# Optimization experiments

Hardware: AMD Instinct MI355X
Metric: run time of the kernel (lower is better)

The kernel has to match this reference:

```python
import jax, jax.numpy as jnp
import numpy as np

EPS_MASK = 1e-6   # clamp eps from DNN_Beamformer __init__
EPS_MVDR = 1e-15  # eps in get_mvdr_vector / psd normalization
SCALING = 2.0     # AttentionReference softmax scaling


def _psd(xs, mask):
    # xs: (B,F,C,T) complex, mask: (B,F,C,T) real -> psd: (B,F,C,C) complex
    m = mask.mean(axis=-2)                                   # (B,F,T)
    m = m / (m.sum(axis=-1, keepdims=True) + EPS_MVDR)
    # sum_t xs[c,t] * conj(xs[e,t]) * m[t], never materializing (B,F,T,C,C)
    return jnp.einsum('bfct,bfet,bft->bfce', xs, xs.conj(), m)


def _attention_reference(psd_in, mlp_w, mlp_b, gvec_w, gvec_b):
    # psd_in: (B,F,C,C) complex -> u: (B,C)
    C = psd_in.shape[-1]
    eye = jnp.eye(C, dtype=bool)
    psd = jnp.where(eye, 0.0, psd_in)                        # zero diagonal
    psd = psd.sum(axis=-1) / (C - 1)                         # (B,F,C)
    psd = jnp.swapaxes(psd, -1, -2)                          # (B,C,F)
    feat = jnp.sqrt(psd.real ** 2 + psd.imag ** 2)           # (B,C,F)
    h = jnp.tanh(feat @ mlp_w + mlp_b)                       # (B,C,att)
    e = (h @ gvec_w + gvec_b)[..., 0]                        # (B,C)
    return jax.nn.softmax(SCALING * e, axis=-1)


def _mvdr_vector(psd_s, psd_n, u):
    # psd_s, psd_n: (B,F,C,C) complex; u: (B,C) real -> ws: (B,F,C) complex
    C = psd_n.shape[-1]
    psd_n = psd_n + EPS_MVDR * jnp.eye(C, dtype=psd_n.dtype)
    numerator = jnp.linalg.solve(psd_n, psd_s)               # inv(psd_n) @ psd_s
    tr = jnp.trace(numerator, axis1=-2, axis2=-1)            # (B,F)
    ws = numerator / (tr[..., None, None] + EPS_MVDR)        # (B,F,C,C)
    return jnp.einsum('bfec,bc->bfe', ws, u.astype(ws.dtype))


def setup_inputs() -> dict:
    key = jax.random.key(0)
    ks = jax.random.split(key, 8)
    B, T, C, F, A = 8, 800, 8, 513, 320
    return {
        'data_real': jax.random.normal(ks[0], (B, T, C, F), jnp.float32),
        'data_imag': jax.random.normal(ks[1], (B, T, C, F), jnp.float32),
        'mask_speech': jax.random.uniform(ks[2], (B, F, C, T), jnp.float32),
        'mask_noise': jax.random.uniform(ks[3], (B, F, C, T), jnp.float32),
        'mlp_w': jax.random.normal(ks[4], (F, A), jnp.float32) / np.sqrt(F),
        'mlp_b': jnp.zeros((A,), jnp.float32),
        'gvec_w': jax.random.normal(ks[5], (A, 1), jnp.float32) / np.sqrt(A),
        'gvec_b': jnp.zeros((1,), jnp.float32),
        'ilens': jnp.full((8,), 800, dtype=jnp.int32),
    }


def reference(data_real, data_imag, mask_speech, mask_noise,
              mlp_w, mlp_b, gvec_w, gvec_b, ilens):
    # data: (B,T,C,F) -> permuted to (B,F,C,T) as in forward
    data = data_real + 1j * data_imag
    x = jnp.transpose(data, (0, 3, 2, 1))                    # (B,F,C,T)
    ms = jnp.maximum(mask_speech, EPS_MASK)
    mn = jnp.maximum(mask_noise, EPS_MASK)
    psd_s = _psd(x, ms)                                      # (B,F,C,C)
    psd_n = _psd(x, mn)                                      # (B,F,C,C)
    u = _attention_reference(psd_s, mlp_w, mlp_b, gvec_w, gvec_b)  # (B,C)
    ws = _mvdr_vector(psd_s, psd_n, u)                       # (B,F,C)
    enhanced = jnp.einsum('bfc,bfct->bft', ws.conj(), x)     # (B,F,T)
    enhanced = jnp.swapaxes(enhanced, -1, -2)                # (B,T,F)
    # return real/imag stacked so the output is a real tensor
    return jnp.stack([enhanced.real, enhanced.imag], axis=-1)
```

## Files before the change

kernel.cpp:

```cpp
#include <hip/hip_runtime.h>
#include <math.h>

#define NB 8
#define NT 800
#define NC 8
#define NF 513
#define NFT 9
#define NTC 16
#define TCHUNK 50
#define NE 146
#define NPAIR 36


__global__ __launch_bounds__(256)
void k_maskred(const float* __restrict__ ms, const float* __restrict__ mn,
               float* __restrict__ mrs, float* __restrict__ mrn) {
  __shared__ float ts[64][65];
  __shared__ float tn[64][65];
  const int tx = threadIdx.x & 63;
  const int wy = threadIdx.x >> 6;
  const int ft = blockIdx.x, tt = blockIdx.y, b = blockIdx.z;
  const int f0 = ft * 64, t0 = tt * 64;
  const int t = t0 + tx;
  const bool tvalid = (t < NT);

  for (int fl = wy; fl < 64; fl += 4) {
    const int f = f0 + fl;
    float as = 0.f, an = 0.f;
    if (f < NF && tvalid) {
      const float* mbs = ms + (((size_t)b * NF + f) * NC) * NT + t;
      const float* mbn = mn + (((size_t)b * NF + f) * NC) * NT + t;
#pragma unroll
      for (int c = 0; c < NC; c++) {
        as += fmaxf(mbs[c * NT], 1e-6f);
        an += fmaxf(mbn[c * NT], 1e-6f);
      }
    }
    ts[fl][tx] = as * 0.125f;
    tn[fl][tx] = an * 0.125f;
  }
  __syncthreads();
  for (int tl = wy; tl < 64; tl += 4) {
    const int tg = t0 + tl, f = f0 + tx;
    if (tg < NT && f < NF) {
      mrs[((size_t)b * NT + tg) * NF + f] = ts[tx][tl];
      mrn[((size_t)b * NT + tg) * NF + f] = tn[tx][tl];
    }
  }
}

__device__ __forceinline__ void accum_psd(const float* __restrict__ drb,
                                          const float* __restrict__ dib, int t,
                                          float m_s, float m_n,
                                          float* __restrict__ sr, float* __restrict__ si,
                                          float* __restrict__ nr, float* __restrict__ ni) {
  float xr[NC], xi[NC];
#pragma unroll
  for (int c = 0; c < NC; c++) {
    xr[c] = drb[(t * NC + c) * NF];
    xi[c] = dib[(t * NC + c) * NF];
  }
  int p = 0;
#pragma unroll
  for (int c = 0; c < NC; c++) {
#pragma unroll
    for (int e = c; e < NC; e++) {
      float pr = xr[c] * xr[e] + xi[c] * xi[e];
      float pi = xi[c] * xr[e] - xr[c] * xi[e];
      sr[p] += m_s * pr; si[p] += m_s * pi;
      nr[p] += m_n * pr; ni[p] += m_n * pi;
      p++;
    }
  }
}

__global__ __launch_bounds__(64, 2)
void k_psd_partial(const float* __restrict__ dr, const float* __restrict__ di,
                   const float* __restrict__ mrs, const float* __restrict__ mrn,
                   float* __restrict__ part) {
  const int fl = threadIdx.x;
  const int ft = blockIdx.x, b = blockIdx.y, tc = blockIdx.z;
  const int f = ft * 64 + fl;

  float sr[NPAIR], si[NPAIR], nr[NPAIR], ni[NPAIR];
#pragma unroll
  for (int p = 0; p < NPAIR; p++) { sr[p] = 0.f; si[p] = 0.f; nr[p] = 0.f; ni[p] = 0.f; }
  float Ss = 0.f, Sn = 0.f;

  if (f < NF) {
    const float* drb  = dr  + (size_t)b * NT * NC * NF + f;
    const float* dib  = di  + (size_t)b * NT * NC * NF + f;
    const float* mrsb = mrs + (size_t)b * NT * NF + f;
    const float* mrnb = mrn + (size_t)b * NT * NF + f;
    const int t0 = tc * TCHUNK;
    for (int tb = 0; tb < TCHUNK; tb += 2) {
      const int t = t0 + tb;
      const float ms0 = mrsb[(size_t)t * NF];
      const float ms1 = mrsb[(size_t)(t + 1) * NF];
      const float mn0 = mrnb[(size_t)t * NF];
      const float mn1 = mrnb[(size_t)(t + 1) * NF];
      Ss += ms0 + ms1; Sn += mn0 + mn1;
      accum_psd(drb, dib, t,     ms0, mn0, sr, si, nr, ni);
      accum_psd(drb, dib, t + 1, ms1, mn1, sr, si, nr, ni);
    }
  }

  float* out = part + (((size_t)(tc * NB + b) * NFT + ft) * NE) * 64 + fl;
#pragma unroll
  for (int p = 0; p < NPAIR; p++) { out[(2 * p) * 64] = sr[p]; out[(2 * p + 1) * 64] = si[p]; }
#pragma unroll
  for (int p = 0; p < NPAIR; p++) { out[(72 + 2 * p) * 64] = nr[p]; out[(72 + 2 * p + 1) * 64] = ni[p]; }
  out[144 * 64] = Ss;
  out[145 * 64] = Sn;
}

__global__ __launch_bounds__(256)
void k_reduce_parts(const float* __restrict__ part, float* __restrict__ comp) {
  const size_t total = (size_t)NB * NFT * NE * 64;
  const size_t idx = (size_t)blockIdx.x * 256 + threadIdx.x;
  if (idx >= total) return;
  const size_t stride = total;
  float s = 0.f;
#pragma unroll
  for (int tc = 0; tc < NTC; tc++) s += part[(size_t)tc * stride + idx];
  comp[idx] = s;
}

__global__ __launch_bounds__(320)
void k_attention(const float* __restrict__ comp,
                 const float* __restrict__ mlp_w, const float* __restrict__ mlp_b,
                 const float* __restrict__ gvec_w, const float* __restrict__ gvec_b,
                 float* __restrict__ e_buf) {
  __shared__ float feat[NF];
  __shared__ float wred[5];
  const int b = blockIdx.x >> 3, c = blockIdx.x & 7;
  const int tid = threadIdx.x;

  for (int f = tid; f < NF; f += 320) {
    const int ft = f >> 6, fl = f & 63;
    const float* base = comp + (((size_t)b * NFT + ft) * NE) * 64 + fl;
    float rs = 0.f, is = 0.f;
#pragma unroll
    for (int e = 0; e < NC; ++e) {
      if (e == c) continue;
      const int lo = (e < c) ? e : c, hi = (e < c) ? c : e;
      const int p = lo * 8 - (lo * (lo + 1)) / 2 + hi;
      rs += base[(2 * p) * 64];
      const float im = base[(2 * p + 1) * 64];
      is += (e > c) ? im : -im;
    }
    const float S = base[144 * 64];
    feat[f] = sqrtf(rs * rs + is * is) / (7.f * (S + 1e-15f));
  }
  __syncthreads();

  const int a = tid;
  float acc = mlp_b[a];
  for (int f = 0; f < NF; ++f) acc = fmaf(feat[f], mlp_w[f * 320 + a], acc);
  float contrib = tanhf(acc) * gvec_w[a];
#pragma unroll
  for (int off = 32; off > 0; off >>= 1) contrib += __shfl_down(contrib, off);
  if ((tid & 63) == 0) wred[tid >> 6] = contrib;
  __syncthreads();
  if (tid == 0) {
    float s = gvec_b[0];
#pragma unroll
    for (int w = 0; w < 5; ++w) s += wred[w];
    e_buf[blockIdx.x] = s;
  }
}

__global__ void k_softmax_u(const float* __restrict__ e_buf, float* __restrict__ u_buf) {
  const int b = threadIdx.x;
  if (b < NB) {
    float v[NC], m = -1e30f;
#pragma unroll
    for (int c = 0; c < NC; c++) { v[c] = 2.f * e_buf[b * 8 + c]; m = fmaxf(m, v[c]); }
    float s = 0.f;
#pragma unroll
    for (int c = 0; c < NC; c++) { v[c] = expf(v[c] - m); s += v[c]; }
    const float inv = 1.f / s;
#pragma unroll
    for (int c = 0; c < NC; c++) u_buf[b * 8 + c] = v[c] * inv;
  }
}

__global__ __launch_bounds__(64, 1)
void k_solve(const float* __restrict__ comp, const float* __restrict__ u_buf,
             float* __restrict__ wsvec) {
  const int fl = threadIdx.x, ft = blockIdx.x, b = blockIdx.y;
  const int f = ft * 64 + fl;
  if (f >= NF) return;
  const float* base = comp + (((size_t)b * NFT + ft) * NE) * 64 + fl;

  float Ar[8][8], Ai[8][8];
#pragma unroll
  for (int j = 0; j < 8; j++) {
#pragma unroll
    for (int i = j; i < 8; i++) {
      const int p = j * 8 - (j * (j + 1)) / 2 + i;
      Ar[i][j] = base[(72 + 2 * p) * 64];
      Ai[i][j] = (i == j) ? 0.f : -base[(72 + 2 * p + 1) * 64];
    }
  }
#pragma unroll
  for (int i = 0; i < 8; i++) Ar[i][i] += 1e-15f;

  float dinv[8];
#pragma unroll
  for (int k = 0; k < 8; k++) {
    const float d = sqrtf(fmaxf(Ar[k][k], 1e-30f));
    const float id = 1.f / d;
    dinv[k] = id;
#pragma unroll
    for (int i = k + 1; i < 8; i++) { Ar[i][k] *= id; Ai[i][k] *= id; }
#pragma unroll
    for (int j = k + 1; j < 8; j++) {
#pragma unroll
      for (int i = j; i < 8; i++) {
        Ar[i][j] -= Ar[i][k] * Ar[j][k] + Ai[i][k] * Ai[j][k];
        Ai[i][j] -= Ai[i][k] * Ar[j][k] - Ar[i][k] * Ai[j][k];
      }
    }
  }

  float trr = 0.f, tri = 0.f;
  float war[8], wai[8];
#pragma unroll
  for (int e = 0; e < 8; e++) { war[e] = 0.f; wai[e] = 0.f; }
  const float* ub = u_buf + b * 8;

#pragma unroll
  for (int c = 0; c < 8; c++) {
    float syr[8], syi[8];
#pragma unroll
    for (int e = 0; e < 8; e++) {
      const int lo = (e < c) ? e : c, hi = (e < c) ? c : e;
      const int p = lo * 8 - (lo * (lo + 1)) / 2 + hi;
      syr[e] = base[(2 * p) * 64];
      const float im = base[(2 * p + 1) * 64];
      syi[e] = (e <= c) ? im : -im;
    }
    float yr[8], yi[8];
#pragma unroll
    for (int i = 0; i < 8; i++) {
      float ar = syr[i], ai = syi[i];
#pragma unroll
      for (int m = 0; m < 8; m++) {
        if (m < i) {
          ar -= Ar[i][m] * yr[m] - Ai[i][m] * yi[m];
          ai -= Ar[i][m] * yi[m] + Ai[i][m] * yr[m];
        }
      }
      yr[i] = ar * dinv[i]; yi[i] = ai * dinv[i];
    }
    float zr[8], zi[8];
#pragma unroll
    for (int i = 7; i >= 0; i--) {
      float ar = yr[i], ai = yi[i];
#pragma unroll
      for (int m = 0; m < 8; m++) {
        if (m > i) {
          ar -= Ar[m][i] * zr[m] + Ai[m][i] * zi[m];
          ai -= Ar[m][i] * zi[m] - Ai[m][i] * zr[m];
        }
      }
      zr[i] = ar * dinv[i]; zi[i] = ai * dinv[i];
    }
    trr += zr[c]; tri += zi[c];
    const float uc = ub[c];
#pragma unroll
    for (int e = 0; e < 8; e++) { war[e] += zr[e] * uc; wai[e] += zi[e] * uc; }
  }

  const float denr = trr + 1e-15f, deni = tri;
  const float inv = 1.f / (denr * denr + deni * deni);
  float2* wv = (float2*)wsvec + ((size_t)b * NF + f) * 8;
#pragma unroll
  for (int e = 0; e < 8; e++) {
    wv[e] = make_float2((war[e] * denr + wai[e] * deni) * inv,
                        (wai[e] * denr - war[e] * deni) * inv);
  }
}

__global__ __launch_bounds__(64)
void k_apply(const float* __restrict__ dr, const float* __restrict__ di,
             const float* __restrict__ wsvec, float* __restrict__ out) {
  const int ft = blockIdx.x, b = blockIdx.y, tt = blockIdx.z;
  const int f = ft * 64 + threadIdx.x;
  if (f >= NF) return;
  float wr[8], wi[8];
  const float2* wv = (const float2*)wsvec + ((size_t)b * NF + f) * 8;
#pragma unroll
  for (int c = 0; c < 8; c++) { float2 w = wv[c]; wr[c] = w.x; wi[c] = w.y; }
  const float* drb = dr + (size_t)b * NT * NC * NF + f;
  const float* dib = di + (size_t)b * NT * NC * NF + f;
  float2* ob = (float2*)out + (size_t)b * NT * NF + f;
  const int t1 = tt * 32 + 32;
  for (int t = tt * 32; t < t1; ++t) {
    float re = 0.f, im = 0.f;
#pragma unroll
    for (int c = 0; c < 8; c++) {
      const float xr = drb[(t * NC + c) * NF];
      const float xi = dib[(t * NC + c) * NF];
      re += wr[c] * xr + wi[c] * xi;
      im += wr[c] * xi - wi[c] * xr;
    }
    ob[(size_t)t * NF] = make_float2(re, im);
  }
}

extern "C" void kernel_launch(void* const* d_in, const int* in_sizes, int n_in,
                              void* d_out, int out_size, void* d_ws, size_t ws_size,
                              hipStream_t stream) {
  const float* dr     = (const float*)d_in[0];
  const float* di     = (const float*)d_in[1];
  const float* msk_s  = (const float*)d_in[2];
  const float* msk_n  = (const float*)d_in[3];
  const float* mlp_w  = (const float*)d_in[4];
  const float* mlp_b  = (const float*)d_in[5];
  const float* gvec_w = (const float*)d_in[6];
  const float* gvec_b = (const float*)d_in[7];

  float* part  = (float*)d_ws;
  float* mrs   = part + (size_t)NTC * NB * NFT * NE * 64;
  float* mrn   = mrs + (size_t)NB * NT * NF;
  float* comp  = mrn + (size_t)NB * NT * NF;
  float* e_buf = comp + (size_t)NB * NFT * NE * 64;
  float* u_buf = e_buf + 64;
  float* wsvec = u_buf + 64;
  float* out   = (float*)d_out;

  k_maskred<<<dim3(NFT, 13, NB), 256, 0, stream>>>(msk_s, msk_n, mrs, mrn);
  k_psd_partial<<<dim3(NFT, NB, NTC), 64, 0, stream>>>(dr, di, mrs, mrn, part);
  {
    const size_t total = (size_t)NB * NFT * NE * 64;
    k_reduce_parts<<<(int)((total + 255) / 256), 256, 0, stream>>>(part, comp);
  }
  k_attention<<<64, 320, 0, stream>>>(comp, mlp_w, mlp_b, gvec_w, gvec_b, e_buf);
  k_softmax_u<<<1, 64, 0, stream>>>(e_buf, u_buf);
  k_solve<<<dim3(NFT, NB), 64, 0, stream>>>(comp, u_buf, wsvec);
  k_apply<<<dim3(NFT, NB, 25), 64, 0, stream>>>(dr, di, wsvec, out);
}
```

Measured before the change: 538.8 us.

## Atomic PSD accumulation, parallel per-column solve, vectorized mask reduce, finer splits

```diff
diff --git a/kernel.cpp b/kernel.cpp
--- a/kernel.cpp
+++ b/kernel.cpp
@@ -6,8 +6,8 @@
 #define NC 8
 #define NF 513
 #define NFT 9
-#define NTC 16
-#define TCHUNK 50
+#define NTC 25
+#define TCHUNK 32
 #define NE 146
 #define NPAIR 36
 
@@ -17,29 +17,39 @@
                float* __restrict__ mrs, float* __restrict__ mrn) {
   __shared__ float ts[64][65];
   __shared__ float tn[64][65];
-  const int tx = threadIdx.x & 63;
-  const int wy = threadIdx.x >> 6;
   const int ft = blockIdx.x, tt = blockIdx.y, b = blockIdx.z;
   const int f0 = ft * 64, t0 = tt * 64;
-  const int t = t0 + tx;
+  const int tq = threadIdx.x & 15;
+  const int fy = threadIdx.x >> 4;
+  const int t = t0 + tq * 4;
   const bool tvalid = (t < NT);
 
-  for (int fl = wy; fl < 64; fl += 4) {
+#pragma unroll
+  for (int p = 0; p < 4; p++) {
+    const int fl = p * 16 + fy;
     const int f = f0 + fl;
-    float as = 0.f, an = 0.f;
+    float4 as = make_float4(0.f, 0.f, 0.f, 0.f);
+    float4 an = make_float4(0.f, 0.f, 0.f, 0.f);
     if (f < NF && tvalid) {
       const float* mbs = ms + (((size_t)b * NF + f) * NC) * NT + t;
       const float* mbn = mn + (((size_t)b * NF + f) * NC) * NT + t;
 #pragma unroll
       for (int c = 0; c < NC; c++) {
-        as += fmaxf(mbs[c * NT], 1e-6f);
-        an += fmaxf(mbn[c * NT], 1e-6f);
+        const float4 a = *(const float4*)(mbs + c * NT);
+        as.x += fmaxf(a.x, 1e-6f); as.y += fmaxf(a.y, 1e-6f);
+        as.z += fmaxf(a.z, 1e-6f); as.w += fmaxf(a.w, 1e-6f);
+        const float4 q = *(const float4*)(mbn + c * NT);
+        an.x += fmaxf(q.x, 1e-6f); an.y += fmaxf(q.y, 1e-6f);
+        an.z += fmaxf(q.z, 1e-6f); an.w += fmaxf(q.w, 1e-6f);
       }
     }
-    ts[fl][tx] = as * 0.125f;
-    tn[fl][tx] = an * 0.125f;
+    ts[fl][tq * 4 + 0] = as.x * 0.125f; ts[fl][tq * 4 + 1] = as.y * 0.125f;
+    ts[fl][tq * 4 + 2] = as.z * 0.125f; ts[fl][tq * 4 + 3] = as.w * 0.125f;
+    tn[fl][tq * 4 + 0] = an.x * 0.125f; tn[fl][tq * 4 + 1] = an.y * 0.125f;
+    tn[fl][tq * 4 + 2] = an.z * 0.125f; tn[fl][tq * 4 + 3] = an.w * 0.125f;
   }
   __syncthreads();
+  const int tx = threadIdx.x & 63, wy = threadIdx.x >> 6;
   for (int tl = wy; tl < 64; tl += 4) {
     const int tg = t0 + tl, f = f0 + tx;
     if (tg < NT && f < NF) {
@@ -75,9 +85,9 @@
 }
 
 __global__ __launch_bounds__(64, 2)
-void k_psd_partial(const float* __restrict__ dr, const float* __restrict__ di,
-                   const float* __restrict__ mrs, const float* __restrict__ mrn,
-                   float* __restrict__ part) {
+void k_psd(const float* __restrict__ dr, const float* __restrict__ di,
+           const float* __restrict__ mrs, const float* __restrict__ mrn,
+           float* __restrict__ comp) {
   const int fl = threadIdx.x;
   const int ft = blockIdx.x, b = blockIdx.y, tc = blockIdx.z;
   const int f = ft * 64 + fl;
@@ -105,25 +115,21 @@
     }
   }
 
-  float* out = part + (((size_t)(tc * NB + b) * NFT + ft) * NE) * 64 + fl;
-#pragma unroll
-  for (int p = 0; p < NPAIR; p++) { out[(2 * p) * 64] = sr[p]; out[(2 * p + 1) * 64] = si[p]; }
-#pragma unroll
-  for (int p = 0; p < NPAIR; p++) { out[(72 + 2 * p) * 64] = nr[p]; out[(72 + 2 * p + 1) * 64] = ni[p]; }
-  out[144 * 64] = Ss;
-  out[145 * 64] = Sn;
-}
-
-__global__ __launch_bounds__(256)
-void k_reduce_parts(const float* __restrict__ part, float* __restrict__ comp) {
-  const size_t total = (size_t)NB * NFT * NE * 64;
-  const size_t idx = (size_t)blockIdx.x * 256 + threadIdx.x;
-  if (idx >= total) return;
-  const size_t stride = total;
-  float s = 0.f;
-#pragma unroll
-  for (int tc = 0; tc < NTC; tc++) s += part[(size_t)tc * stride + idx];
-  comp[idx] = s;
+  float* out = comp + (((size_t)b * NFT + ft) * NE) * 64 + fl;
+  if (f < NF) {
+#pragma unroll
+    for (int p = 0; p < NPAIR; p++) {
+      unsafeAtomicAdd(&out[(2 * p) * 64], sr[p]);
+      unsafeAtomicAdd(&out[(2 * p + 1) * 64], si[p]);
+    }
+#pragma unroll
+    for (int p = 0; p < NPAIR; p++) {
+      unsafeAtomicAdd(&out[(72 + 2 * p) * 64], nr[p]);
+      unsafeAtomicAdd(&out[(72 + 2 * p + 1) * 64], ni[p]);
+    }
+    unsafeAtomicAdd(&out[144 * 64], Ss);
+    unsafeAtomicAdd(&out[145 * 64], Sn);
+  }
 }
 
 __global__ __launch_bounds__(320)
@@ -170,27 +176,15 @@
   }
 }
 
-__global__ void k_softmax_u(const float* __restrict__ e_buf, float* __restrict__ u_buf) {
-  const int b = threadIdx.x;
-  if (b < NB) {
-    float v[NC], m = -1e30f;
-#pragma unroll
-    for (int c = 0; c < NC; c++) { v[c] = 2.f * e_buf[b * 8 + c]; m = fmaxf(m, v[c]); }
-    float s = 0.f;
-#pragma unroll
-    for (int c = 0; c < NC; c++) { v[c] = expf(v[c] - m); s += v[c]; }
-    const float inv = 1.f / s;
-#pragma unroll
-    for (int c = 0; c < NC; c++) u_buf[b * 8 + c] = v[c] * inv;
-  }
-}
-
-__global__ __launch_bounds__(64, 1)
-void k_solve(const float* __restrict__ comp, const float* __restrict__ u_buf,
+__global__ __launch_bounds__(64)
+void k_solve(const float* __restrict__ comp, const float* __restrict__ e_buf,
              float* __restrict__ wsvec) {
-  const int fl = threadIdx.x, ft = blockIdx.x, b = blockIdx.y;
-  const int f = ft * 64 + fl;
+  const int lane = threadIdx.x;
+  const int c = lane & 7, fsub = lane >> 3;
+  const int b = blockIdx.y;
+  const int f = blockIdx.x * 8 + fsub;
   if (f >= NF) return;
+  const int ft = f >> 6, fl = f & 63;
   const float* base = comp + (((size_t)b * NFT + ft) * NE) * 64 + fl;
 
   float Ar[8][8], Ai[8][8];
@@ -224,63 +218,69 @@
     }
   }
 
-  float trr = 0.f, tri = 0.f;
-  float war[8], wai[8];
-#pragma unroll
-  for (int e = 0; e < 8; e++) { war[e] = 0.f; wai[e] = 0.f; }
-  const float* ub = u_buf + b * 8;
-
-#pragma unroll
-  for (int c = 0; c < 8; c++) {
-    float syr[8], syi[8];
+  float syr[8], syi[8];
+#pragma unroll
+  for (int e = 0; e < 8; e++) {
+    const int lo = (e < c) ? e : c, hi = (e < c) ? c : e;
+    const int p = lo * 8 - (lo * (lo + 1)) / 2 + hi;
+    syr[e] = base[(2 * p) * 64];
+    const float im = base[(2 * p + 1) * 64];
+    syi[e] = (e <= c) ? im : -im;
+  }
+  float yr[8], yi[8];
+#pragma unroll
+  for (int i = 0; i < 8; i++) {
+    float ar = syr[i], ai = syi[i];
+#pragma unroll
+    for (int m = 0; m < 8; m++) {
+      if (m < i) {
+        ar -= Ar[i][m] * yr[m] - Ai[i][m] * yi[m];
+        ai -= Ar[i][m] * yi[m] + Ai[i][m] * yr[m];
+      }
+    }
+    yr[i] = ar * dinv[i]; yi[i] = ai * dinv[i];
+  }
+  float zr[8], zi[8];
+#pragma unroll
+  for (int i = 7; i >= 0; i--) {
+    float ar = yr[i], ai = yi[i];
+#pragma unroll
+    for (int m = 0; m < 8; m++) {
+      if (m > i) {
+        ar -= Ar[m][i] * zr[m] + Ai[m][i] * zi[m];
+        ai -= Ar[m][i] * zi[m] - Ai[m][i] * zr[m];
+      }
+    }
+    zr[i] = ar * dinv[i]; zi[i] = ai * dinv[i];
+  }
+
+  float ev[8], mx = -1e30f;
+#pragma unroll
+  for (int j = 0; j < 8; j++) { ev[j] = 2.f * e_buf[b * 8 + j]; mx = fmaxf(mx, ev[j]); }
+  float ssum = 0.f;
+#pragma unroll
+  for (int j = 0; j < 8; j++) ssum += expf(ev[j] - mx);
+  const float uc = expf(ev[c] - mx) / ssum;
+
+  float trr = zr[c], tri = zi[c];
+  float wr[8], wi[8];
+#pragma unroll
+  for (int e = 0; e < 8; e++) { wr[e] = zr[e] * uc; wi[e] = zi[e] * uc; }
+#pragma unroll
+  for (int m = 1; m <= 4; m <<= 1) {
+    trr += __shfl_xor(trr, m); tri += __shfl_xor(tri, m);
 #pragma unroll
     for (int e = 0; e < 8; e++) {
-      const int lo = (e < c) ? e : c, hi = (e < c) ? c : e;
-      const int p = lo * 8 - (lo * (lo + 1)) / 2 + hi;
-      syr[e] = base[(2 * p) * 64];
-      const float im = base[(2 * p + 1) * 64];
-      syi[e] = (e <= c) ? im : -im;
-    }
-    float yr[8], yi[8];
-#pragma unroll
-    for (int i = 0; i < 8; i++) {
-      float ar = syr[i], ai = syi[i];
-#pragma unroll
-      for (int m = 0; m < 8; m++) {
-        if (m < i) {
-          ar -= Ar[i][m] * yr[m] - Ai[i][m] * yi[m];
-          ai -= Ar[i][m] * yi[m] + Ai[i][m] * yr[m];
-        }
-      }
-      yr[i] = ar * dinv[i]; yi[i] = ai * dinv[i];
-    }
-    float zr[8], zi[8];
-#pragma unroll
-    for (int i = 7; i >= 0; i--) {
-      float ar = yr[i], ai = yi[i];
-#pragma unroll
-      for (int m = 0; m < 8; m++) {
-        if (m > i) {
-          ar -= Ar[m][i] * zr[m] + Ai[m][i] * zi[m];
-          ai -= Ar[m][i] * zi[m] - Ai[m][i] * zr[m];
-        }
-      }
-      zr[i] = ar * dinv[i]; zi[i] = ai * dinv[i];
-    }
-    trr += zr[c]; tri += zi[c];
-    const float uc = ub[c];
-#pragma unroll
-    for (int e = 0; e < 8; e++) { war[e] += zr[e] * uc; wai[e] += zi[e] * uc; }
+      wr[e] += __shfl_xor(wr[e], m);
+      wi[e] += __shfl_xor(wi[e], m);
+    }
   }
 
   const float denr = trr + 1e-15f, deni = tri;
   const float inv = 1.f / (denr * denr + deni * deni);
   float2* wv = (float2*)wsvec + ((size_t)b * NF + f) * 8;
-#pragma unroll
-  for (int e = 0; e < 8; e++) {
-    wv[e] = make_float2((war[e] * denr + wai[e] * deni) * inv,
-                        (wai[e] * denr - war[e] * deni) * inv);
-  }
+  wv[c] = make_float2((wr[c] * denr + wi[c] * deni) * inv,
+                      (wi[c] * denr - wr[c] * deni) * inv);
 }
 
 __global__ __launch_bounds__(64)
@@ -296,8 +296,8 @@
   const float* drb = dr + (size_t)b * NT * NC * NF + f;
   const float* dib = di + (size_t)b * NT * NC * NF + f;
   float2* ob = (float2*)out + (size_t)b * NT * NF + f;
-  const int t1 = tt * 32 + 32;
-  for (int t = tt * 32; t < t1; ++t) {
+  const int t1 = tt * 16 + 16;
+  for (int t = tt * 16; t < t1; ++t) {
     float re = 0.f, im = 0.f;
 #pragma unroll
     for (int c = 0; c < 8; c++) {
@@ -322,23 +322,17 @@
   const float* gvec_w = (const float*)d_in[6];
   const float* gvec_b = (const float*)d_in[7];
 
-  float* part  = (float*)d_ws;
-  float* mrs   = part + (size_t)NTC * NB * NFT * NE * 64;
+  float* mrs   = (float*)d_ws;
   float* mrn   = mrs + (size_t)NB * NT * NF;
   float* comp  = mrn + (size_t)NB * NT * NF;
   float* e_buf = comp + (size_t)NB * NFT * NE * 64;
-  float* u_buf = e_buf + 64;
-  float* wsvec = u_buf + 64;
+  float* wsvec = e_buf + 64;
   float* out   = (float*)d_out;
 
+  hipMemsetAsync(comp, 0, (size_t)NB * NFT * NE * 64 * sizeof(float), stream);
   k_maskred<<<dim3(NFT, 13, NB), 256, 0, stream>>>(msk_s, msk_n, mrs, mrn);
-  k_psd_partial<<<dim3(NFT, NB, NTC), 64, 0, stream>>>(dr, di, mrs, mrn, part);
-  {
-    const size_t total = (size_t)NB * NFT * NE * 64;
-    k_reduce_parts<<<(int)((total + 255) / 256), 256, 0, stream>>>(part, comp);
-  }
+  k_psd<<<dim3(NFT, NB, NTC), 64, 0, stream>>>(dr, di, mrs, mrn, comp);
   k_attention<<<64, 320, 0, stream>>>(comp, mlp_w, mlp_b, gvec_w, gvec_b, e_buf);
-  k_softmax_u<<<1, 64, 0, stream>>>(e_buf, u_buf);
-  k_solve<<<dim3(NFT, NB), 64, 0, stream>>>(comp, u_buf, wsvec);
-  k_apply<<<dim3(NFT, NB, 25), 64, 0, stream>>>(dr, di, wsvec, out);
-}
+  k_solve<<<dim3(65, NB), 64, 0, stream>>>(comp, e_buf, wsvec);
+  k_apply<<<dim3(NFT, NB, 50), 64, 0, stream>>>(dr, di, wsvec, out);
+}
```

Result: faster. 522.6 us (-3.0%).
